# Performance work log

Measured on AMD Instinct MI355X. Metric: run time of the kernel, lower is better.

## Reference

```python
import jax, jax.numpy as jnp
from jax import lax
import numpy as np

# static config (matches init_kwargs)
B, H, Wd, C = 32, 96, 96, 64
nW, K, PAD = 4, 3, 1
WS = 48  # window_size = H // sqrt(nW)


def setup_inputs() -> dict:
    key = jax.random.key(0)
    ks = jax.random.split(key, 24)
    def p(i, shape, s=0.02):
        return jax.random.normal(ks[i], shape, dtype=jnp.float32) * s
    return {
        "x": jax.random.normal(ks[0], (B, H * Wd, C), dtype=jnp.float32),
        # se: conv1x1 -> gelu -> conv1x1 -> sigmoid
        "se_w1": p(1, (C, C)), "se_b1": p(2, (C,)),
        "se_w2": p(3, (C, C)), "se_b2": p(4, (C,)),
        # WinKernel_Reweight
        "dc_w": p(5, (nW, C)), "dc_b": p(6, (nW,)),            # grouped 1x1, nW groups of C->1
        "l1_w": p(7, (4 * nW, nW)), "l1_b": p(8, (4 * nW,)),
        "l2_w": p(9, (nW, 4 * nW)), "l2_b": p(10, (nW,)),
        # gk_fusion: grouped 1x1 (dim groups, nW->1 per group)
        "gkf_w": p(11, (C, nW)), "gkf_b": p(12, (C,)),
        # Fusion (gk_sum)
        "fu_proj_w": p(13, (C, nW, nW)), "fu_proj_b": p(14, (C * nW,)),  # grouped 1x1, dim groups of nW->nW
        "fu_fc1_w": p(15, (C, nW * C)), "fu_fc1_b": p(16, (C,)),
        "fu_fc2_w": p(17, (nW * C, C)), "fu_fc2_b": p(18, (nW * C,)),
        "fu_po_w": p(19, (C, C)), "fu_po_b": p(20, (C,)),
        # final proj_out
        "po_w": p(21, (C, C)), "po_b": p(22, (C,)),
    }


def _gelu(t):
    return jax.nn.gelu(t, approximate=False)  # torch nn.GELU default = exact erf


def _conv1x1(w, b, t):
    return jnp.einsum('oi,bihw->bohw', w, t) + b[None, :, None, None]


def _forward(x, se_w1, se_b1, se_w2, se_b2, dc_w, dc_b, l1_w, l1_b, l2_w, l2_b,
             gkf_w, gkf_b, fu_proj_w, fu_proj_b, fu_fc1_w, fu_fc1_b,
             fu_fc2_w, fu_fc2_b, fu_po_w, fu_po_b, po_w, po_b):
    xh = x.reshape(B, H, Wd, C)
    # window_partition -> (B*nW, C, WS, WS), windows row-major within each batch element
    win = (xh.reshape(B, 2, WS, 2, WS, C)
             .transpose(0, 1, 3, 2, 4, 5)
             .reshape(B * nW, WS, WS, C)
             .transpose(0, 3, 1, 2))
    # adaptive avg pool (WS->K, exact since WS % K == 0)
    pool = WS // K
    kern = win.reshape(B * nW, C, K, pool, K, pool).mean(axis=(3, 5))  # (B*nW, C, K, K)
    # SE block replaces kernels
    kern_se = jax.nn.sigmoid(_conv1x1(se_w2, se_b2, _gelu(_conv1x1(se_w1, se_b1, kern))))
    # WinKernel_Reweight
    xwin = win.reshape(B, nW * C, WS, WS)
    ww = xwin.mean(axis=(2, 3)).reshape(B, nW, C)                 # GAP then grouped 1x1 (nW groups)
    ww = jnp.einsum('wc,bwc->bw', dc_w, ww) + dc_b                # (B, nW)
    ww = _gelu(ww @ l1_w.T + l1_b)
    ww = jax.nn.sigmoid(ww @ l2_w.T + l2_b)                       # (B, nW)
    kr = kern_se.reshape(B, nW, C, K, K) * ww[:, :, None, None, None]
    # gk_fusion: after transpose(1,2) channel order is c-major; grouped conv -> per-c mix over windows
    gkf = jnp.einsum('cw,bwcij->bcij', gkf_w, kr) + gkf_b[None, :, None, None]  # (B, C, K, K)
    # Fusion (gk_sum) on SE kernels (window-major channel layout)
    feats_in = kern_se.reshape(B, nW * C, K, K)
    fg = feats_in.reshape(B, C, nW, K, K)                         # groups = consecutive nW channels
    feats = _gelu(jnp.einsum('goi,bgikl->bgokl', fu_proj_w, fg)
                  + fu_proj_b.reshape(1, C, nW, 1, 1))
    v = feats.mean(axis=(3, 4)).reshape(B, C * nW)                # GAP
    v = _gelu(v @ fu_fc1_w.T + fu_fc1_b)                          # (B, C)
    av = jax.nn.softmax((v @ fu_fc2_w.T + fu_fc2_b).reshape(B, nW, C), axis=1)
    x_sum = jnp.einsum('bwckl,bwc->bckl', feats_in.reshape(B, nW, C, K, K), av)
    gks = gkf + _conv1x1(fu_po_w, fu_po_b, x_sum)                 # (B, C, K, K)
    # assemble per-(sample, kernel-branch, channel) depthwise kernels and convolve
    gk = jnp.stack([gkf, gks], axis=1).reshape(B * 2 * C, 1, K, K)
    xi = jnp.broadcast_to(xh.transpose(0, 3, 1, 2)[:, None], (B, 2, C, H, Wd))
    xi = xi.reshape(1, B * 2 * C, H, Wd)
    y = lax.conv_general_dilated(xi, gk, window_strides=(1, 1),
                                 padding=((PAD, PAD), (PAD, PAD)),
                                 feature_group_count=B * 2 * C,
                                 dimension_numbers=('NCHW', 'OIHW', 'NCHW'))
    y = y.reshape(B, 2, C, H, Wd).sum(axis=1)                     # sum the two kernel branches
    y = _conv1x1(po_w, po_b, y)
    return y.transpose(0, 2, 3, 1).reshape(B, H * Wd, C)


def reference(x, se_w1, se_b1, se_w2, se_b2, dc_w, dc_b, l1_w, l1_b, l2_w, l2_b,
              gkf_w, gkf_b, fu_proj_w, fu_proj_b, fu_fc1_w, fu_fc1_b,
              fu_fc2_w, fu_fc2_b, fu_po_w, fu_po_b, po_w, po_b):
    return _forward(x, se_w1, se_b1, se_w2, se_b2, dc_w, dc_b, l1_w, l1_b, l2_w, l2_b,
                    gkf_w, gkf_b, fu_proj_w, fu_proj_b, fu_fc1_w, fu_fc1_b,
                    fu_fc2_w, fu_fc2_b, fu_po_w, fu_po_b, po_w, po_b)
```

## Files before the change

kernel.cpp:

```cpp
#include <hip/hip_runtime.h>
#include <hip/hip_bf16.h>

#define NPIX 9216

typedef __attribute__((ext_vector_type(8))) short short8v;
typedef __attribute__((ext_vector_type(4))) float floatx4;

__device__ __forceinline__ float geluf(float x){
  return 0.5f * x * (1.0f + erff(x * 0.70710678118654752440f));
}
__device__ __forceinline__ float sigm(float x){
  return 1.0f / (1.0f + expf(-x));
}
__device__ __forceinline__ unsigned short f2bf(float f){
  __hip_bfloat16 h = __float2bfloat16(f);
  return *(unsigned short*)&h;
}

__global__ __launch_bounds__(256) void k_pool(const float* __restrict__ x,
                                              float* __restrict__ kern)
{
  int blk = blockIdx.x;
  int bw = blk / 9, rem = blk % 9;
  int ki = rem / 3, kj = rem % 3;
  int b = bw >> 2, w = bw & 3;
  int wr = w >> 1, wc = w & 1;
  int t = threadIdx.x;
  int cg = t & 15, rw = t >> 4;
  int h = wr*48 + ki*16 + rw;
  int col0 = wc*48 + kj*16;
  size_t base = ((size_t)(b*NPIX + h*96 + col0))*64 + cg*4;
  float a0=0.f,a1=0.f,a2=0.f,a3=0.f;
  #pragma unroll
  for (int j=0;j<16;j++){
    float4 u = *(const float4*)(x + base + (size_t)j*64);
    a0 += u.x; a1 += u.y; a2 += u.z; a3 += u.w;
  }
  __shared__ float red[16*64];
  float* rr = &red[rw*64 + cg*4];
  rr[0]=a0; rr[1]=a1; rr[2]=a2; rr[3]=a3;
  __syncthreads();
  if (t < 64){
    float s = 0.f;
    #pragma unroll
    for (int r=0;r<16;r++) s += red[r*64 + t];
    kern[(size_t)bw*576 + t*9 + rem] = s * (1.0f/256.0f);
  }
}

__global__ __launch_bounds__(256) void k_se(const float* __restrict__ kern_ws,
    const float* __restrict__ se_w1, const float* __restrict__ se_b1,
    const float* __restrict__ se_w2, const float* __restrict__ se_b2,
    const float* __restrict__ po_w,
    float* __restrict__ kse_ws, float* __restrict__ wwc_ws,
    unsigned short* __restrict__ frag_pw)
{
  int bw = blockIdx.x;
  int t = threadIdx.x;
  __shared__ float s_w1[64*65];
  __shared__ float s_w2[64*65];
  __shared__ float s_kern[64*13];
  __shared__ float s_t2[64*13];

  if (bw == 0){
    for (int idx=t; idx<4096; idx+=256){
      int f = idx >> 9, L = (idx >> 3) & 63, j = idx & 7;
      int nb = f >> 1, kb = f & 1;
      int o = nb*16 + (L & 15);
      int c = kb*32 + ((L >> 4) & 3)*8 + j;
      frag_pw[idx] = f2bf(po_w[o*64 + c]);
    }
  }
  for (int idx=t; idx<576; idx+=256){
    int c = idx/9, p = idx%9;
    s_kern[c*13+p] = kern_ws[bw*576 + idx];
  }
  for (int j=t; j<4096; j+=256){
    int o=j>>6, i=j&63;
    s_w1[i*65+o] = se_w1[j];
    s_w2[i*65+o] = se_w2[j];
  }
  __syncthreads();
  for (int idx=t; idx<576; idx+=256){
    int o = idx & 63, p = idx >> 6;
    float acc = se_b1[o];
    #pragma unroll 8
    for (int i=0;i<64;i++) acc += s_w1[i*65+o]*s_kern[i*13+p];
    s_t2[o*13+p] = geluf(acc);
  }
  __syncthreads();
  for (int idx=t; idx<576; idx+=256){
    int o = idx & 63, p = idx >> 6;
    float acc = se_b2[o];
    #pragma unroll 8
    for (int i=0;i<64;i++) acc += s_w2[i*65+o]*s_t2[i*13+p];
    kse_ws[bw*576 + o*9 + p] = sigm(acc);
  }
  if (t < 64){
    const float* kr = &s_kern[t*13];
    float s = kr[0]+kr[1]+kr[2]+kr[3]+kr[4]+kr[5]+kr[6]+kr[7]+kr[8];
    wwc_ws[bw*64 + t] = s * (1.0f/9.0f);
  }
}

__global__ __launch_bounds__(256) void k_rest(const float* __restrict__ kse_ws,
    const float* __restrict__ wwc_ws,
    const float* __restrict__ dc_w,  const float* __restrict__ dc_b,
    const float* __restrict__ l1_w,  const float* __restrict__ l1_b,
    const float* __restrict__ l2_w,  const float* __restrict__ l2_b,
    const float* __restrict__ gkf_w, const float* __restrict__ gkf_b,
    const float* __restrict__ fu_proj_w, const float* __restrict__ fu_proj_b,
    const float* __restrict__ fu_fc1_w,  const float* __restrict__ fu_fc1_b,
    const float* __restrict__ fu_fc2_w,  const float* __restrict__ fu_fc2_b,
    const float* __restrict__ fu_po_w,   const float* __restrict__ fu_po_b,
    float* __restrict__ kc_ws)
{
  int b = blockIdx.x;
  int t = threadIdx.x;
  int lane = t & 63, wv = t >> 6;

  __shared__ float s_kse[2304];
  __shared__ float s_wwc[256];
  __shared__ float s_pow[64*65];
  __shared__ float s_prj[1088];
  __shared__ float s_feats[2304];
  __shared__ float s_gkf[576];
  __shared__ float s_xsum[576];
  __shared__ float s_v0[256];
  __shared__ float s_av[256];
  __shared__ float s_v1[64];
  __shared__ float s_small[64];

  for (int idx=t; idx<2304; idx+=256) s_kse[idx] = kse_ws[b*2304 + idx];
  s_wwc[t] = wwc_ws[b*256 + t];
  for (int j=t; j<4096; j+=256){ int c=j>>6, i=j&63; s_pow[i*65+c] = fu_po_w[j]; }
  for (int j=t; j<1024; j+=256){ int g=j>>4, oi=j&15; s_prj[g*17+oi] = fu_proj_w[j]; }
  __syncthreads();

  for (int idx=t; idx<2304; idx+=256){
    int g = idx & 63, op = idx >> 6;
    int o = op / 9, p = op % 9;
    float acc = fu_proj_b[g*4+o];
    #pragma unroll
    for (int i=0;i<4;i++){
      int ch = g*4+i;
      acc += s_prj[g*17 + o*4 + i] * s_kse[(ch>>6)*576 + (ch&63)*9 + p];
    }
    s_feats[(g*4+o)*9 + p] = geluf(acc);
  }
  if (t<4){
    float acc = dc_b[t];
    #pragma unroll 8
    for (int c=0;c<64;c++) acc += dc_w[t*64+c]*s_wwc[t*64+c];
    s_small[t] = acc;
  }
  __syncthreads();

  {
    const float* f = &s_feats[t*9];
    s_v0[t] = (f[0]+f[1]+f[2]+f[3]+f[4]+f[5]+f[6]+f[7]+f[8]) * (1.0f/9.0f);
  }
  if (t<16){
    float acc = l1_b[t];
    #pragma unroll
    for (int w=0;w<4;w++) acc += l1_w[t*4+w]*s_small[w];
    s_small[16+t] = geluf(acc);
  }
  __syncthreads();

  if (t<4){
    float acc = l2_b[t];
    #pragma unroll
    for (int j=0;j<16;j++) acc += l2_w[t*16+j]*s_small[16+j];
    s_small[32+t] = sigm(acc);
  }
  {
    #pragma unroll
    for (int oi=0; oi<16; oi++){
      int o = wv*16 + oi;
      float v = fu_fc1_w[o*256 +       lane] * s_v0[      lane]
              + fu_fc1_w[o*256 +  64 + lane] * s_v0[ 64 + lane]
              + fu_fc1_w[o*256 + 128 + lane] * s_v0[128 + lane]
              + fu_fc1_w[o*256 + 192 + lane] * s_v0[192 + lane];
      #pragma unroll
      for (int m=32; m>0; m>>=1) v += __shfl_xor(v, m);
      if (lane == 0) s_v1[o] = geluf(v + fu_fc1_b[o]);
    }
  }
  __syncthreads();

  {
    const float4* wr = (const float4*)(fu_fc2_w + t*64);
    float acc = 0.f;
    #pragma unroll
    for (int q=0;q<16;q++){
      float4 wq = wr[q];
      acc += wq.x*s_v1[q*4] + wq.y*s_v1[q*4+1] + wq.z*s_v1[q*4+2] + wq.w*s_v1[q*4+3];
    }
    s_av[t] = acc + fu_fc2_b[t];
  }
  for (int idx=t; idx<576; idx+=256){
    int c = idx & 63, p = idx >> 6;
    float acc = gkf_b[c];
    #pragma unroll
    for (int w=0;w<4;w++) acc += gkf_w[c*4+w]*s_kse[w*576+c*9+p]*s_small[32+w];
    s_gkf[c*9+p] = acc;
  }
  __syncthreads();

  if (t<64){
    float z0=s_av[t], z1=s_av[64+t], z2=s_av[128+t], z3=s_av[192+t];
    float mx = fmaxf(fmaxf(z0,z1),fmaxf(z2,z3));
    float e0=expf(z0-mx), e1=expf(z1-mx), e2=expf(z2-mx), e3=expf(z3-mx);
    float inv = 1.0f/(e0+e1+e2+e3);
    s_av[t]=e0*inv; s_av[64+t]=e1*inv; s_av[128+t]=e2*inv; s_av[192+t]=e3*inv;
  }
  __syncthreads();

  for (int idx=t; idx<576; idx+=256){
    int c = idx & 63, p = idx >> 6;
    float s=0.f;
    #pragma unroll
    for (int w=0;w<4;w++) s += s_kse[w*576+c*9+p]*s_av[w*64+c];
    s_xsum[c*9+p] = s;
  }
  __syncthreads();

  for (int idx=t; idx<576; idx+=256){
    int c = idx & 63, p = idx >> 6;
    float acc = 2.0f*s_gkf[c*9+p] + fu_po_b[c];
    #pragma unroll 8
    for (int i=0;i<64;i++) acc += s_pow[i*65+c]*s_xsum[i*9+p];
    kc_ws[b*576 + c*9 + p] = acc;
  }
}

__global__ __launch_bounds__(256, 4) void k_conv(const float* __restrict__ x,
                                                 const float* __restrict__ kc_ws,
                                                 const unsigned short* __restrict__ frag_pw,
                                                 const float* __restrict__ po_b,
                                                 float* __restrict__ out)
{
  int bi = blockIdx.x;
  int b = bi / 144, tile = bi % 144;
  int th = tile / 12, tw = tile % 12;
  int h0 = th*8, w0 = tw*8;
  int t = threadIdx.x;

  __shared__ float s_x[100*64];
  __shared__ unsigned short s_tmp[64*72];
  __shared__ float s_kc[576];

  for (int idx=t; idx<1600; idx+=256){
    int pix = idx >> 4, c4 = idx & 15;
    int r = pix / 10, col = pix % 10;
    int hh = h0 - 1 + r, ww = w0 - 1 + col;
    float4 v = make_float4(0.f,0.f,0.f,0.f);
    if (hh >= 0 && hh < 96 && ww >= 0 && ww < 96)
      v = *(const float4*)(x + (((size_t)b*NPIX + hh*96 + ww)<<6) + c4*4);
    *(float4*)&s_x[pix*64 + c4*4] = v;
  }
  for (int idx=t; idx<576; idx+=256) s_kc[idx] = kc_ws[b*576 + idx];
  __syncthreads();

  {
    int c = t & 63, rg = t >> 6;
    int r0 = rg*2;
    float k0=s_kc[c*9+0],k1=s_kc[c*9+1],k2=s_kc[c*9+2],
          k3=s_kc[c*9+3],k4=s_kc[c*9+4],k5=s_kc[c*9+5],
          k6=s_kc[c*9+6],k7=s_kc[c*9+7],k8=s_kc[c*9+8];
    float row[4][10];
    #pragma unroll
    for (int rr=0; rr<4; rr++)
      #pragma unroll
      for (int cc=0; cc<10; cc++)
        row[rr][cc] = s_x[((r0+rr)*10 + cc)*64 + c];
    #pragma unroll
    for (int dr=0; dr<2; dr++){
      int pr = r0 + dr;
      #pragma unroll
      for (int pc=0; pc<8; pc++){
        float acc = k0*row[dr+0][pc] + k1*row[dr+0][pc+1] + k2*row[dr+0][pc+2]
                  + k3*row[dr+1][pc] + k4*row[dr+1][pc+1] + k5*row[dr+1][pc+2]
                  + k6*row[dr+2][pc] + k7*row[dr+2][pc+1] + k8*row[dr+2][pc+2];
        s_tmp[(pr*8 + pc)*72 + c] = f2bf(acc);
      }
    }
  }
  __syncthreads();

  {
    int wv = t >> 6, lane = t & 63;
    int m = wv*16 + (lane & 15);
    int quad = lane >> 4;
    floatx4 acc[4] = {{0.f,0.f,0.f,0.f},{0.f,0.f,0.f,0.f},
                      {0.f,0.f,0.f,0.f},{0.f,0.f,0.f,0.f}};
    #pragma unroll
    for (int kb=0; kb<2; kb++){
      short8v afrag = *(const short8v*)&s_tmp[m*72 + kb*32 + quad*8];
      #pragma unroll
      for (int nb=0; nb<4; nb++){
        short8v bfrag = *(const short8v*)(frag_pw + (nb*2+kb)*512 + lane*8);
        acc[nb] = __builtin_amdgcn_mfma_f32_16x16x32_bf16(afrag, bfrag, acc[nb], 0, 0, 0);
      }
    }
    #pragma unroll
    for (int nb=0; nb<4; nb++){
      int o = nb*16 + (lane & 15);
      float pb = po_b[o];
      #pragma unroll
      for (int r=0; r<4; r++){
        int px = wv*16 + quad*4 + r;
        int hh = h0 + (px >> 3), wwp = w0 + (px & 7);
        out[(((size_t)b*NPIX + hh*96 + wwp)<<6) + o] = acc[nb][r] + pb;
      }
    }
  }
}

extern "C" void kernel_launch(void* const* d_in, const int* in_sizes, int n_in,
                              void* d_out, int out_size, void* d_ws, size_t ws_size,
                              hipStream_t stream) {
  const float* x        = (const float*)d_in[0];
  const float* se_w1    = (const float*)d_in[1];
  const float* se_b1    = (const float*)d_in[2];
  const float* se_w2    = (const float*)d_in[3];
  const float* se_b2    = (const float*)d_in[4];
  const float* dc_w     = (const float*)d_in[5];
  const float* dc_b     = (const float*)d_in[6];
  const float* l1_w     = (const float*)d_in[7];
  const float* l1_b     = (const float*)d_in[8];
  const float* l2_w     = (const float*)d_in[9];
  const float* l2_b     = (const float*)d_in[10];
  const float* gkf_w    = (const float*)d_in[11];
  const float* gkf_b    = (const float*)d_in[12];
  const float* fu_proj_w= (const float*)d_in[13];
  const float* fu_proj_b= (const float*)d_in[14];
  const float* fu_fc1_w = (const float*)d_in[15];
  const float* fu_fc1_b = (const float*)d_in[16];
  const float* fu_fc2_w = (const float*)d_in[17];
  const float* fu_fc2_b = (const float*)d_in[18];
  const float* fu_po_w  = (const float*)d_in[19];
  const float* fu_po_b  = (const float*)d_in[20];
  const float* po_w     = (const float*)d_in[21];
  const float* po_b     = (const float*)d_in[22];

  float* kern_ws = (float*)d_ws;
  float* kc_ws   = kern_ws + 73728;
  unsigned short* frag_pw = (unsigned short*)(kc_ws + 18432);
  float* kse_ws  = kc_ws + 18432 + 2048;
  float* wwc_ws  = kse_ws + 73728;

  k_pool<<<1152, 256, 0, stream>>>(x, kern_ws);
  k_se<<<128, 256, 0, stream>>>(kern_ws, se_w1, se_b1, se_w2, se_b2, po_w,
                                kse_ws, wwc_ws, frag_pw);
  k_rest<<<32, 256, 0, stream>>>(kse_ws, wwc_ws,
                                 dc_w, dc_b, l1_w, l1_b, l2_w, l2_b,
                                 gkf_w, gkf_b, fu_proj_w, fu_proj_b,
                                 fu_fc1_w, fu_fc1_b, fu_fc2_w, fu_fc2_b,
                                 fu_po_w, fu_po_b, kc_ws);
  k_conv<<<4608, 256, 0, stream>>>(x, kc_ws, frag_pw, po_b, (float*)d_out);
}
```

Before: 236.6 us.

## Fuse SE and per-batch kernel stages into one 512-thread kernel

Merges the SE block kernel and the per-batch reweight/fusion kernel into a single 512-thread kernel per batch element. Intermediate SE results stay in shared memory instead of making a workspace round trip, and one launch is removed. The bf16 weight-fragment prep moves into the pool kernel. The conv kernel also gets a fast unguarded halo load for interior tiles and uses nontemporal output stores. The trade-off is that only 32 blocks now run the SE math, where 128 blocks ran it before, and shared-memory use per block grows.

```diff
diff --git a/kernel.cpp b/kernel.cpp
--- a/kernel.cpp
+++ b/kernel.cpp
@@ -18,14 +18,25 @@
 }
 
 __global__ __launch_bounds__(256) void k_pool(const float* __restrict__ x,
-                                              float* __restrict__ kern)
+                                              const float* __restrict__ po_w,
+                                              float* __restrict__ kern,
+                                              unsigned short* __restrict__ frag_pw)
 {
   int blk = blockIdx.x;
+  int t = threadIdx.x;
+  if (blk == 0){
+    for (int idx=t; idx<4096; idx+=256){
+      int f = idx >> 9, L = (idx >> 3) & 63, j = idx & 7;
+      int nb = f >> 1, kb = f & 1;
+      int o = nb*16 + (L & 15);
+      int c = kb*32 + ((L >> 4) & 3)*8 + j;
+      frag_pw[idx] = f2bf(po_w[o*64 + c]);
+    }
+  }
   int bw = blk / 9, rem = blk % 9;
   int ki = rem / 3, kj = rem % 3;
   int b = bw >> 2, w = bw & 3;
   int wr = w >> 1, wc = w & 1;
-  int t = threadIdx.x;
   int cg = t & 15, rw = t >> 4;
   int h = wr*48 + ki*16 + rw;
   int col0 = wc*48 + kj*16;
@@ -48,63 +59,9 @@
   }
 }
 
-__global__ __launch_bounds__(256) void k_se(const float* __restrict__ kern_ws,
+__global__ __launch_bounds__(512) void k_fuse(const float* __restrict__ kern_ws,
     const float* __restrict__ se_w1, const float* __restrict__ se_b1,
     const float* __restrict__ se_w2, const float* __restrict__ se_b2,
-    const float* __restrict__ po_w,
-    float* __restrict__ kse_ws, float* __restrict__ wwc_ws,
-    unsigned short* __restrict__ frag_pw)
-{
-  int bw = blockIdx.x;
-  int t = threadIdx.x;
-  __shared__ float s_w1[64*65];
-  __shared__ float s_w2[64*65];
-  __shared__ float s_kern[64*13];
-  __shared__ float s_t2[64*13];
-
-  if (bw == 0){
-    for (int idx=t; idx<4096; idx+=256){
-      int f = idx >> 9, L = (idx >> 3) & 63, j = idx & 7;
-      int nb = f >> 1, kb = f & 1;
-      int o = nb*16 + (L & 15);
-      int c = kb*32 + ((L >> 4) & 3)*8 + j;
-      frag_pw[idx] = f2bf(po_w[o*64 + c]);
-    }
-  }
-  for (int idx=t; idx<576; idx+=256){
-    int c = idx/9, p = idx%9;
-    s_kern[c*13+p] = kern_ws[bw*576 + idx];
-  }
-  for (int j=t; j<4096; j+=256){
-    int o=j>>6, i=j&63;
-    s_w1[i*65+o] = se_w1[j];
-    s_w2[i*65+o] = se_w2[j];
-  }
-  __syncthreads();
-  for (int idx=t; idx<576; idx+=256){
-    int o = idx & 63, p = idx >> 6;
-    float acc = se_b1[o];
-    #pragma unroll 8
-    for (int i=0;i<64;i++) acc += s_w1[i*65+o]*s_kern[i*13+p];
-    s_t2[o*13+p] = geluf(acc);
-  }
-  __syncthreads();
-  for (int idx=t; idx<576; idx+=256){
-    int o = idx & 63, p = idx >> 6;
-    float acc = se_b2[o];
-    #pragma unroll 8
-    for (int i=0;i<64;i++) acc += s_w2[i*65+o]*s_t2[i*13+p];
-    kse_ws[bw*576 + o*9 + p] = sigm(acc);
-  }
-  if (t < 64){
-    const float* kr = &s_kern[t*13];
-    float s = kr[0]+kr[1]+kr[2]+kr[3]+kr[4]+kr[5]+kr[6]+kr[7]+kr[8];
-    wwc_ws[bw*64 + t] = s * (1.0f/9.0f);
-  }
-}
-
-__global__ __launch_bounds__(256) void k_rest(const float* __restrict__ kse_ws,
-    const float* __restrict__ wwc_ws,
     const float* __restrict__ dc_w,  const float* __restrict__ dc_b,
     const float* __restrict__ l1_w,  const float* __restrict__ l1_b,
     const float* __restrict__ l2_w,  const float* __restrict__ l2_b,
@@ -119,36 +76,60 @@
   int t = threadIdx.x;
   int lane = t & 63, wv = t >> 6;
 
+  __shared__ float s_w1[64*65];
+  __shared__ float s_w2[64*65];
+  __shared__ float s_pow[64*65];
+  __shared__ float s_kern[4*64*13];
+  __shared__ float s_t1[4*64*13];
   __shared__ float s_kse[2304];
-  __shared__ float s_wwc[256];
-  __shared__ float s_pow[64*65];
   __shared__ float s_prj[1088];
   __shared__ float s_feats[2304];
   __shared__ float s_gkf[576];
   __shared__ float s_xsum[576];
+  __shared__ float s_wwc[256];
   __shared__ float s_v0[256];
   __shared__ float s_av[256];
   __shared__ float s_v1[64];
   __shared__ float s_small[64];
 
-  for (int idx=t; idx<2304; idx+=256) s_kse[idx] = kse_ws[b*2304 + idx];
-  s_wwc[t] = wwc_ws[b*256 + t];
-  for (int j=t; j<4096; j+=256){ int c=j>>6, i=j&63; s_pow[i*65+c] = fu_po_w[j]; }
-  for (int j=t; j<1024; j+=256){ int g=j>>4, oi=j&15; s_prj[g*17+oi] = fu_proj_w[j]; }
-  __syncthreads();
-
-  for (int idx=t; idx<2304; idx+=256){
-    int g = idx & 63, op = idx >> 6;
-    int o = op / 9, p = op % 9;
-    float acc = fu_proj_b[g*4+o];
-    #pragma unroll
-    for (int i=0;i<4;i++){
-      int ch = g*4+i;
-      acc += s_prj[g*17 + o*4 + i] * s_kse[(ch>>6)*576 + (ch&63)*9 + p];
-    }
-    s_feats[(g*4+o)*9 + p] = geluf(acc);
-  }
-  if (t<4){
+  for (int idx=t; idx<2304; idx+=512){
+    int w = idx/576, cp = idx - w*576;
+    int c = cp/9, p = cp - c*9;
+    s_kern[(w*64+c)*13+p] = kern_ws[(size_t)(b*4+w)*576 + cp];
+  }
+  for (int j=t; j<4096; j+=512){
+    int o=j>>6, i=j&63;
+    s_w1[i*65+o]  = se_w1[j];
+    s_w2[i*65+o]  = se_w2[j];
+    s_pow[i*65+o] = fu_po_w[j];
+  }
+  for (int j=t; j<1024; j+=512){ int g=j>>4, oi=j&15; s_prj[g*17+oi] = fu_proj_w[j]; }
+  __syncthreads();
+
+  for (int idx=t; idx<2304; idx+=512){
+    int o = idx & 63, wp = idx >> 6;
+    int w = wp/9, p = wp - w*9;
+    float acc = se_b1[o];
+    #pragma unroll 8
+    for (int i=0;i<64;i++) acc += s_w1[i*65+o]*s_kern[(w*64+i)*13+p];
+    s_t1[(w*64+o)*13+p] = geluf(acc);
+  }
+  if (t < 256){
+    const float* kr = &s_kern[t*13];
+    float s = kr[0]+kr[1]+kr[2]+kr[3]+kr[4]+kr[5]+kr[6]+kr[7]+kr[8];
+    s_wwc[t] = s * (1.0f/9.0f);
+  }
+  __syncthreads();
+
+  for (int idx=t; idx<2304; idx+=512){
+    int o = idx & 63, wp = idx >> 6;
+    int w = wp/9, p = wp - w*9;
+    float acc = se_b2[o];
+    #pragma unroll 8
+    for (int i=0;i<64;i++) acc += s_w2[i*65+o]*s_t1[(w*64+i)*13+p];
+    s_kse[w*576 + o*9 + p] = sigm(acc);
+  }
+  if (t < 4){
     float acc = dc_b[t];
     #pragma unroll 8
     for (int c=0;c<64;c++) acc += dc_w[t*64+c]*s_wwc[t*64+c];
@@ -156,40 +137,51 @@
   }
   __syncthreads();
 
-  {
+  for (int idx=t; idx<2304; idx+=512){
+    int g = idx & 63, op = idx >> 6;
+    int o = op/9, p = op - o*9;
+    float acc = fu_proj_b[g*4+o];
+    #pragma unroll
+    for (int i=0;i<4;i++){
+      int ch = g*4+i;
+      acc += s_prj[g*17 + o*4 + i] * s_kse[(ch>>6)*576 + (ch&63)*9 + p];
+    }
+    s_feats[(g*4+o)*9 + p] = geluf(acc);
+  }
+  if (t < 16){
+    float acc = l1_b[t];
+    #pragma unroll
+    for (int w=0;w<4;w++) acc += l1_w[t*4+w]*s_small[w];
+    s_small[16+t] = geluf(acc);
+  }
+  __syncthreads();
+
+  if (t < 256){
     const float* f = &s_feats[t*9];
     s_v0[t] = (f[0]+f[1]+f[2]+f[3]+f[4]+f[5]+f[6]+f[7]+f[8]) * (1.0f/9.0f);
-  }
-  if (t<16){
-    float acc = l1_b[t];
-    #pragma unroll
-    for (int w=0;w<4;w++) acc += l1_w[t*4+w]*s_small[w];
-    s_small[16+t] = geluf(acc);
-  }
-  __syncthreads();
-
-  if (t<4){
-    float acc = l2_b[t];
-    #pragma unroll
-    for (int j=0;j<16;j++) acc += l2_w[t*16+j]*s_small[16+j];
-    s_small[32+t] = sigm(acc);
-  }
-  {
-    #pragma unroll
-    for (int oi=0; oi<16; oi++){
-      int o = wv*16 + oi;
-      float v = fu_fc1_w[o*256 +       lane] * s_v0[      lane]
-              + fu_fc1_w[o*256 +  64 + lane] * s_v0[ 64 + lane]
-              + fu_fc1_w[o*256 + 128 + lane] * s_v0[128 + lane]
-              + fu_fc1_w[o*256 + 192 + lane] * s_v0[192 + lane];
-      #pragma unroll
-      for (int m=32; m>0; m>>=1) v += __shfl_xor(v, m);
-      if (lane == 0) s_v1[o] = geluf(v + fu_fc1_b[o]);
-    }
-  }
-  __syncthreads();
-
-  {
+  } else if (t < 260){
+    int tt = t - 256;
+    float acc = l2_b[tt];
+    #pragma unroll
+    for (int j=0;j<16;j++) acc += l2_w[tt*16+j]*s_small[16+j];
+    s_small[32+tt] = sigm(acc);
+  }
+  __syncthreads();
+
+  #pragma unroll
+  for (int oi=0; oi<8; oi++){
+    int o = wv*8 + oi;
+    float v = fu_fc1_w[o*256 +       lane] * s_v0[      lane]
+            + fu_fc1_w[o*256 +  64 + lane] * s_v0[ 64 + lane]
+            + fu_fc1_w[o*256 + 128 + lane] * s_v0[128 + lane]
+            + fu_fc1_w[o*256 + 192 + lane] * s_v0[192 + lane];
+    #pragma unroll
+    for (int m=32; m>0; m>>=1) v += __shfl_xor(v, m);
+    if (lane == 0) s_v1[o] = geluf(v + fu_fc1_b[o]);
+  }
+  __syncthreads();
+
+  if (t < 256){
     const float4* wr = (const float4*)(fu_fc2_w + t*64);
     float acc = 0.f;
     #pragma unroll
@@ -199,7 +191,7 @@
     }
     s_av[t] = acc + fu_fc2_b[t];
   }
-  for (int idx=t; idx<576; idx+=256){
+  for (int idx=t; idx<576; idx+=512){
     int c = idx & 63, p = idx >> 6;
     float acc = gkf_b[c];
     #pragma unroll
@@ -208,7 +200,7 @@
   }
   __syncthreads();
 
-  if (t<64){
+  if (t < 64){
     float z0=s_av[t], z1=s_av[64+t], z2=s_av[128+t], z3=s_av[192+t];
     float mx = fmaxf(fmaxf(z0,z1),fmaxf(z2,z3));
     float e0=expf(z0-mx), e1=expf(z1-mx), e2=expf(z2-mx), e3=expf(z3-mx);
@@ -217,7 +209,7 @@
   }
   __syncthreads();
 
-  for (int idx=t; idx<576; idx+=256){
+  for (int idx=t; idx<576; idx+=512){
     int c = idx & 63, p = idx >> 6;
     float s=0.f;
     #pragma unroll
@@ -226,12 +218,12 @@
   }
   __syncthreads();
 
-  for (int idx=t; idx<576; idx+=256){
+  for (int idx=t; idx<576; idx+=512){
     int c = idx & 63, p = idx >> 6;
     float acc = 2.0f*s_gkf[c*9+p] + fu_po_b[c];
     #pragma unroll 8
     for (int i=0;i<64;i++) acc += s_pow[i*65+c]*s_xsum[i*9+p];
-    kc_ws[b*576 + c*9 + p] = acc;
+    kc_ws[(size_t)b*576 + c*9 + p] = acc;
   }
 }
 
@@ -251,14 +243,24 @@
   __shared__ unsigned short s_tmp[64*72];
   __shared__ float s_kc[576];
 
-  for (int idx=t; idx<1600; idx+=256){
-    int pix = idx >> 4, c4 = idx & 15;
-    int r = pix / 10, col = pix % 10;
-    int hh = h0 - 1 + r, ww = w0 - 1 + col;
-    float4 v = make_float4(0.f,0.f,0.f,0.f);
-    if (hh >= 0 && hh < 96 && ww >= 0 && ww < 96)
-      v = *(const float4*)(x + (((size_t)b*NPIX + hh*96 + ww)<<6) + c4*4);
-    *(float4*)&s_x[pix*64 + c4*4] = v;
+  if (th > 0 && th < 11 && tw > 0 && tw < 11){
+    const float* xb = x + (((size_t)(b*NPIX + (h0-1)*96 + (w0-1)))<<6);
+    for (int idx=t; idx<1600; idx+=256){
+      int pix = idx >> 4, c4 = idx & 15;
+      int r = pix / 10, col = pix - r*10;
+      *(float4*)&s_x[pix*64 + c4*4] =
+        *(const float4*)(xb + (((size_t)(r*96 + col))<<6) + c4*4);
+    }
+  } else {
+    for (int idx=t; idx<1600; idx+=256){
+      int pix = idx >> 4, c4 = idx & 15;
+      int r = pix / 10, col = pix % 10;
+      int hh = h0 - 1 + r, ww = w0 - 1 + col;
+      float4 v = make_float4(0.f,0.f,0.f,0.f);
+      if (hh >= 0 && hh < 96 && ww >= 0 && ww < 96)
+        v = *(const float4*)(x + (((size_t)b*NPIX + hh*96 + ww)<<6) + c4*4);
+      *(float4*)&s_x[pix*64 + c4*4] = v;
+    }
   }
   for (int idx=t; idx<576; idx+=256) s_kc[idx] = kc_ws[b*576 + idx];
   __syncthreads();
@@ -312,7 +314,8 @@
       for (int r=0; r<4; r++){
         int px = wv*16 + quad*4 + r;
         int hh = h0 + (px >> 3), wwp = w0 + (px & 7);
-        out[(((size_t)b*NPIX + hh*96 + wwp)<<6) + o] = acc[nb][r] + pb;
+        __builtin_nontemporal_store(acc[nb][r] + pb,
+            out + (((size_t)b*NPIX + hh*96 + wwp)<<6) + o);
       }
     }
   }
@@ -348,13 +351,10 @@
   float* kern_ws = (float*)d_ws;
   float* kc_ws   = kern_ws + 73728;
   unsigned short* frag_pw = (unsigned short*)(kc_ws + 18432);
-  float* kse_ws  = kc_ws + 18432 + 2048;
-  float* wwc_ws  = kse_ws + 73728;
-
-  k_pool<<<1152, 256, 0, stream>>>(x, kern_ws);
-  k_se<<<128, 256, 0, stream>>>(kern_ws, se_w1, se_b1, se_w2, se_b2, po_w,
-                                kse_ws, wwc_ws, frag_pw);
-  k_rest<<<32, 256, 0, stream>>>(kse_ws, wwc_ws,
+
+  k_pool<<<1152, 256, 0, stream>>>(x, po_w, kern_ws, frag_pw);
+  k_fuse<<<32, 512, 0, stream>>>(kern_ws,
+                                 se_w1, se_b1, se_w2, se_b2,
                                  dc_w, dc_b, l1_w, l1_b, l2_w, l2_b,
                                  gkf_w, gkf_b, fu_proj_w, fu_proj_b,
                                  fu_fc1_w, fu_fc1_b, fu_fc2_w, fu_fc2_b,
```

Result: faster. 230.2 us (-2.7%).
